# Optimization experiments

Hardware: AMD Instinct MI355X
Metric: run time of the kernel (lower is better)

The kernel has to match this reference:

```python
import jax, jax.numpy as jnp
import numpy as np

B, D, H, W = 64, 64, 32, 32
K = 1024  # num_embeddings


def setup_inputs() -> dict:
    key = jax.random.key(0)
    kx, ke = jax.random.split(key)
    x = jax.random.normal(kx, (B, D, H, W), dtype=jnp.float32)
    # original init: uniform(-sqrt(3), sqrt(3)); randn is fine numerically, but
    # we match the original init distribution for fidelity
    limit = 3.0 ** 0.5
    embedding_table = jax.random.uniform(ke, (D, K), dtype=jnp.float32,
                                         minval=-limit, maxval=limit)
    return {"x": x, "embedding_table": embedding_table}


def reference(x, embedding_table):
    b, d, h, w = x.shape
    flat_x = x.transpose(0, 2, 3, 1).reshape(-1, d)            # [N, D]
    distances = ((flat_x ** 2).sum(1, keepdims=True)
                 - 2.0 * flat_x @ embedding_table
                 + (embedding_table ** 2).sum(0, keepdims=True))  # [N, K]
    encoding_indices = jnp.argmin(distances, axis=1)            # [N]
    quantized = embedding_table.T[encoding_indices]             # [N, D] gather
    quantized = quantized.reshape(b, h, w, d).transpose(0, 3, 1, 2)  # [B,D,H,W]
    dictionary_loss = jnp.mean((jax.lax.stop_gradient(x) - quantized) ** 2)
    commitment_loss = jnp.mean((x - jax.lax.stop_gradient(quantized)) ** 2)
    quantized_st = x + jax.lax.stop_gradient(quantized - x)     # straight-through
    return (quantized_st, dictionary_loss, commitment_loss,
            encoding_indices.reshape(b, -1))
```

## Files before the change

kernel.cpp:

```cpp
#include <hip/hip_runtime.h>


#define DDIM 64
#define KNUM 1024
#define HWN  1024
#define EPS  0.02f

typedef __attribute__((ext_vector_type(8))) short short8v;
typedef __attribute__((ext_vector_type(4))) float f32x4;

__device__ __forceinline__ unsigned short bf16_rn(float v) {
    unsigned u = __float_as_uint(v);
    return (unsigned short)((u + 0x7FFFu + ((u >> 16) & 1u)) >> 16);
}
__device__ __forceinline__ float bf16f(unsigned short h) {
    return __uint_as_float(((unsigned)h) << 16);
}

__global__ __launch_bounds__(256) void vq_convert_e(const float* __restrict__ E,
                                                    float* __restrict__ esq,
                                                    unsigned short* __restrict__ eh,
                                                    unsigned short* __restrict__ el) {
    int k = blockIdx.x * 256 + threadIdx.x;
    float s = 0.f;
    #pragma unroll 8
    for (int d = 0; d < DDIM; ++d) {
        float v = E[d * KNUM + k];
        s = fmaf(v, v, s);
        unsigned short h = bf16_rn(v);
        float lo = v - bf16f(h);
        eh[k * DDIM + d] = h;
        el[k * DDIM + d] = bf16_rn(lo);
    }
    esq[k] = s;
}

__global__ __launch_bounds__(256, 2) void vq_mfma_kernel(const float* __restrict__ x,
                                                         const unsigned short* __restrict__ eh,
                                                         const unsigned short* __restrict__ el,
                                                         const float* __restrict__ esq,
                                                         float* __restrict__ oidx) {
    __shared__ unsigned short blds[2][16384];

    const int t = threadIdx.x;
    const int wv = t >> 6, l = t & 63;
    const int m = l & 15, g = l >> 4;
    const int tileBase = blockIdx.x * 8 + wv * 2;

    const int sr   = wv * 8 + (l >> 3);
    const int sc   = (l & 7) * 16;
    const int scsw = sc ^ ((sr & 7) << 4);
    const unsigned short* srcrow0 =
        (sr < 16) ? (eh + (size_t)sr * DDIM + (scsw >> 1))
                  : (el + (size_t)(sr - 16) * DDIM + (scsw >> 1));
    #define STAGEPH(BUF, P)                                                                  \
        _Pragma("unroll")                                                                    \
        for (int q = 0; q < 8; ++q)                                                          \
            __builtin_amdgcn_global_load_lds(                                                \
                (const __attribute__((address_space(1))) void*)(srcrow0 + (size_t)((P) * 8 + q) * 16 * DDIM), \
                (__attribute__((address_space(3))) void*)&blds[BUF][q * 2048 + wv * 512 + l * 8], \
                16, 0, 0);

    short8v axh[2][2], axl[2][2];
    #pragma unroll
    for (int T = 0; T < 2; ++T) {
        const int n0 = (tileBase + T) * 16;
        const int bb = n0 >> 10, hw0 = n0 & 1023;
        const float* xg = x + (size_t)bb * (DDIM * HWN) + hw0 + m;
        #pragma unroll
        for (int s = 0; s < 2; ++s) {
            #pragma unroll
            for (int i = 0; i < 8; ++i) {
                float v = xg[(s * 32 + g * 8 + i) * HWN];
                unsigned short h = bf16_rn(v);
                axh[T][s][i] = (short)h;
                axl[T][s][i] = (short)bf16_rn(v - bf16f(h));
            }
        }
    }

    const int off_h0 = (m * 128 + (((g * 16)     ) ^ ((m & 7) << 4))) >> 1;
    const int off_h1 = (m * 128 + (((64 + g * 16)) ^ ((m & 7) << 4))) >> 1;
    const int off_l0 = off_h0 + 1024;
    const int off_l1 = off_h1 + 1024;

    float min1[2][4], min2[2][4]; int bk[2][4];
    #pragma unroll
    for (int T = 0; T < 2; ++T)
        #pragma unroll
        for (int j = 0; j < 4; ++j) { min1[T][j] = 3.4e38f; min2[T][j] = 3.4e38f; bk[T][j] = 0; }

    STAGEPH(0, 0);
    __syncthreads();

    for (int p = 0; p < 8; ++p) {
        const int cur = p & 1;
        if (p < 7) STAGEPH(cur ^ 1, p + 1);

        #pragma unroll
        for (int ktl = 0; ktl < 8; ++ktl) {
            const int kt = p * 8 + ktl;
            const unsigned short* bb = &blds[cur][ktl * 2048];
            const short8v bh0 = *reinterpret_cast<const short8v*>(bb + off_h0);
            const short8v bh1 = *reinterpret_cast<const short8v*>(bb + off_h1);
            const short8v bl0 = *reinterpret_cast<const short8v*>(bb + off_l0);
            const short8v bl1 = *reinterpret_cast<const short8v*>(bb + off_l1);
            const float esqv = esq[kt * 16 + m];

            #pragma unroll
            for (int T = 0; T < 2; ++T) {
                f32x4 accA = {0.f, 0.f, 0.f, 0.f};
                f32x4 accB = {0.f, 0.f, 0.f, 0.f};
                accA = __builtin_amdgcn_mfma_f32_16x16x32_bf16(axh[T][0], bh0, accA, 0, 0, 0);
                accA = __builtin_amdgcn_mfma_f32_16x16x32_bf16(axh[T][1], bh1, accA, 0, 0, 0);
                accB = __builtin_amdgcn_mfma_f32_16x16x32_bf16(axh[T][0], bl0, accB, 0, 0, 0);
                accB = __builtin_amdgcn_mfma_f32_16x16x32_bf16(axh[T][1], bl1, accB, 0, 0, 0);
                accA = __builtin_amdgcn_mfma_f32_16x16x32_bf16(axl[T][0], bh0, accA, 0, 0, 0);
                accA = __builtin_amdgcn_mfma_f32_16x16x32_bf16(axl[T][1], bh1, accA, 0, 0, 0);
                #pragma unroll
                for (int j = 0; j < 4; ++j) {
                    float dist = fmaf(-2.f, accA[j] + accB[j], esqv);
                    bool lt = dist < min1[T][j];
                    min2[T][j] = lt ? min1[T][j] : fminf(min2[T][j], dist);
                    bk[T][j]   = lt ? (kt * 16 + m) : bk[T][j];
                    min1[T][j] = lt ? dist          : min1[T][j];
                }
            }
        }
        __syncthreads();
    }
    #undef STAGEPH

    #pragma unroll
    for (int T = 0; T < 2; ++T)
        #pragma unroll
        for (int j = 0; j < 4; ++j) {
            float m1 = min1[T][j], m2 = min2[T][j]; int k1 = bk[T][j];
            #pragma unroll
            for (int off = 8; off >= 1; off >>= 1) {
                float om1 = __shfl_xor(m1, off, 16);
                float om2 = __shfl_xor(m2, off, 16);
                int   ok1 = __shfl_xor(k1, off, 16);
                if (om1 < m1 || (om1 == m1 && ok1 < k1)) {
                    m2 = fminf(m1, om2); m1 = om1; k1 = ok1;
                } else {
                    m2 = fminf(m2, fminf(om1, om2) == om1 ? om2 : om1);
                    m2 = fminf(m2, om1 == m1 ? om2 : om1);
                }
            }
            if (m == j) {
                int n = (tileBase + T) * 16 + g * 4 + j;
                bool flag = (m2 - m1) < EPS;
                oidx[n] = flag ? -(float)(k1 + 1) : (float)k1;
            }
        }
}

__global__ __launch_bounds__(256) void vq_epilogue(const float* __restrict__ x,
                                                   const float* __restrict__ E,
                                                   const float* __restrict__ esq,
                                                   float* __restrict__ oidx,
                                                   float* __restrict__ out_q,
                                                   float* __restrict__ partial) {
    __shared__ float xlds[DDIM * 64];
    __shared__ int   klds[64];
    __shared__ float redlds[4];
    const int t  = threadIdx.x;
    const int wv = t >> 6, ln = t & 63;
    const int n0 = blockIdx.x * 64;
    const int b  = n0 >> 10, hw0 = n0 & 1023;
    const float* xbase = x + (size_t)b * (DDIM * HWN) + hw0;
    #pragma unroll
    for (int it = 0; it < 4; ++it) {
        int dbase = it * 16 + wv * 4;
        int dsub  = ln >> 4;
        int off   = (ln & 15) * 4;
        const float* g = xbase + (dbase + dsub) * HWN + off;
        __builtin_amdgcn_global_load_lds(
            (const __attribute__((address_space(1))) void*)g,
            (__attribute__((address_space(3))) void*)&xlds[dbase * 64 + ln * 4],
            16, 0, 0);
    }
    __syncthreads();
    if (t < 64) klds[t] = (int)oidx[n0 + t];
    __syncthreads();

    for (int r = wv; r < 64; r += 4) {
        if (klds[r] >= 0) continue;
        float acc[16];
        #pragma unroll
        for (int kk = 0; kk < 16; ++kk) acc[kk] = 0.f;
        for (int d = 0; d < DDIM; ++d) {
            float xd = xlds[d * 64 + r];
            #pragma unroll
            for (int kk = 0; kk < 16; ++kk)
                acc[kk] = fmaf(xd, E[d * KNUM + kk * 64 + ln], acc[kk]);
        }
        float bm = 3.4e38f; int bkk = KNUM;
        #pragma unroll
        for (int kk = 0; kk < 16; ++kk) {
            int k = kk * 64 + ln;
            float dist = fmaf(-2.f, acc[kk], esq[k]);
            if (dist < bm) { bm = dist; bkk = k; }
        }
        #pragma unroll
        for (int off = 32; off >= 1; off >>= 1) {
            float ob = __shfl_xor(bm, off);
            int   ok = __shfl_xor(bkk, off);
            if (ob < bm || (ob == bm && ok < bkk)) { bm = ob; bkk = ok; }
        }
        if (ln == 0) { klds[r] = bkk; oidx[n0 + r] = (float)bkk; }
    }
    __syncthreads();

    float lsum = 0.f;
    float* outbase = out_q + (size_t)b * (DDIM * HWN) + hw0;
    #pragma unroll 4
    for (int it = 0; it < 16; ++it) {
        int d = it * 4 + (t >> 6);
        int r = t & 63;
        int k = klds[r];
        float q  = E[d * KNUM + k];
        float xv = xlds[d * 64 + r];
        float diff = xv - q;
        lsum = fmaf(diff, diff, lsum);
        outbase[d * HWN + r] = q;
    }
    #pragma unroll
    for (int off = 32; off >= 1; off >>= 1)
        lsum += __shfl_xor(lsum, off);
    if ((t & 63) == 0) redlds[t >> 6] = lsum;
    __syncthreads();
    if (t == 0)
        partial[blockIdx.x] = (redlds[0] + redlds[1]) + (redlds[2] + redlds[3]);
}

__global__ __launch_bounds__(256) void vq_loss_kernel(const float* __restrict__ partial,
                                                      float* __restrict__ out_loss) {
    __shared__ float red[4];
    int t = threadIdx.x;
    float s = 0.f;
    #pragma unroll
    for (int it = 0; it < 4; ++it) s += partial[it * 256 + t];
    #pragma unroll
    for (int off = 32; off >= 1; off >>= 1) s += __shfl_xor(s, off);
    if ((t & 63) == 0) red[t >> 6] = s;
    __syncthreads();
    if (t == 0) {
        float loss = ((red[0] + red[1]) + (red[2] + red[3])) / 4194304.f;
        out_loss[0] = loss;
        out_loss[1] = loss;
    }
}

extern "C" void kernel_launch(void* const* d_in, const int* in_sizes, int n_in,
                              void* d_out, int out_size, void* d_ws, size_t ws_size,
                              hipStream_t stream) {
    const float* x = (const float*)d_in[0];
    const float* E = (const float*)d_in[1];
    float* out      = (float*)d_out;
    float* out_q    = out;
    float* out_loss = out + 4194304;
    float* oidx     = out + 4194306;

    float* esq     = (float*)d_ws;
    float* partial = esq + 1024;
    unsigned short* eh = (unsigned short*)(partial + 1024);
    unsigned short* el = eh + KNUM * DDIM;

    vq_convert_e<<<4, 256, 0, stream>>>(E, esq, eh, el);
    vq_mfma_kernel<<<512, 256, 0, stream>>>(x, eh, el, esq, oidx);
    vq_epilogue<<<1024, 256, 0, stream>>>(x, E, esq, oidx, out_q, partial);
    vq_loss_kernel<<<1, 256, 0, stream>>>(partial, out_loss);
}
```

Measured before the change: 74.13 us.

## Fuse MFMA distance search with epilogue into one kernel per 64-row block

Merges the MFMA nearest-code search kernel and the epilogue (ambiguous-row fp32 recheck, gather, loss partials) into a single kernel. Each block now handles 64 rows, one 16-row tile per wave. Indices are passed through LDS instead of a global round trip, and the x staging buffer reuses the codebook LDS. The change also halves the LDS stage size, raises the occupancy hint to 4 blocks, and folds the two accumulators into one chain with a branchless min update. The cost is that each wave reuses each codebook tile for one row tile instead of two, so more LDS reads are spent per MFMA.

```diff
diff --git a/kernel.cpp b/kernel.cpp
--- a/kernel.cpp
+++ b/kernel.cpp
@@ -35,46 +35,52 @@
     esq[k] = s;
 }
 
-__global__ __launch_bounds__(256, 2) void vq_mfma_kernel(const float* __restrict__ x,
-                                                         const unsigned short* __restrict__ eh,
-                                                         const unsigned short* __restrict__ el,
-                                                         const float* __restrict__ esq,
-                                                         float* __restrict__ oidx) {
-    __shared__ unsigned short blds[2][16384];
+__global__ __launch_bounds__(256, 4) void vq_mfma_fused(const float* __restrict__ x,
+                                                        const float* __restrict__ E,
+                                                        const unsigned short* __restrict__ eh,
+                                                        const unsigned short* __restrict__ el,
+                                                        const float* __restrict__ esq,
+                                                        float* __restrict__ oidx,
+                                                        float* __restrict__ out_q,
+                                                        float* __restrict__ partial) {
+    __shared__ unsigned short blds[2][8192];
+    __shared__ int   klds[64];
+    __shared__ float redlds[4];
 
     const int t = threadIdx.x;
     const int wv = t >> 6, l = t & 63;
     const int m = l & 15, g = l >> 4;
-    const int tileBase = blockIdx.x * 8 + wv * 2;
-
-    const int sr   = wv * 8 + (l >> 3);
-    const int sc   = (l & 7) * 16;
+    const int tile = blockIdx.x * 4 + wv;
+    const int n0 = blockIdx.x * 64;
+    const int b  = n0 >> 10, hw0 = n0 & 1023;
+
+    const int sr   = t >> 3;
+    const int sc   = (t & 7) * 16;
     const int scsw = sc ^ ((sr & 7) << 4);
     const unsigned short* srcrow0 =
         (sr < 16) ? (eh + (size_t)sr * DDIM + (scsw >> 1))
                   : (el + (size_t)(sr - 16) * DDIM + (scsw >> 1));
     #define STAGEPH(BUF, P)                                                                  \
         _Pragma("unroll")                                                                    \
-        for (int q = 0; q < 8; ++q)                                                          \
+        for (int q = 0; q < 4; ++q)                                                          \
             __builtin_amdgcn_global_load_lds(                                                \
-                (const __attribute__((address_space(1))) void*)(srcrow0 + (size_t)((P) * 8 + q) * 16 * DDIM), \
-                (__attribute__((address_space(3))) void*)&blds[BUF][q * 2048 + wv * 512 + l * 8], \
+                (const __attribute__((address_space(1))) void*)(srcrow0 + (size_t)((P) * 4 + q) * 16 * DDIM), \
+                (__attribute__((address_space(3))) void*)&blds[BUF][q * 2048 + t * 8],       \
                 16, 0, 0);
 
-    short8v axh[2][2], axl[2][2];
-    #pragma unroll
-    for (int T = 0; T < 2; ++T) {
-        const int n0 = (tileBase + T) * 16;
-        const int bb = n0 >> 10, hw0 = n0 & 1023;
-        const float* xg = x + (size_t)bb * (DDIM * HWN) + hw0 + m;
+    short8v axh[2], axl[2];
+    {
+        const int tn0 = tile * 16;
+        const int tb = tn0 >> 10, thw = tn0 & 1023;
+        const float* xg = x + (size_t)tb * (DDIM * HWN) + thw + m;
         #pragma unroll
         for (int s = 0; s < 2; ++s) {
             #pragma unroll
             for (int i = 0; i < 8; ++i) {
                 float v = xg[(s * 32 + g * 8 + i) * HWN];
                 unsigned short h = bf16_rn(v);
-                axh[T][s][i] = (short)h;
-                axl[T][s][i] = (short)bf16_rn(v - bf16f(h));
+                axh[s][i] = (short)h;
+                axl[s][i] = (short)bf16_rn(v - bf16f(h));
             }
         }
     }
@@ -84,22 +90,22 @@
     const int off_l0 = off_h0 + 1024;
     const int off_l1 = off_h1 + 1024;
 
-    float min1[2][4], min2[2][4]; int bk[2][4];
-    #pragma unroll
-    for (int T = 0; T < 2; ++T)
-        #pragma unroll
-        for (int j = 0; j < 4; ++j) { min1[T][j] = 3.4e38f; min2[T][j] = 3.4e38f; bk[T][j] = 0; }
+    float min1[4], min2[4]; int bk[4];
+    #pragma unroll
+    for (int j = 0; j < 4; ++j) { min1[j] = 3.4e38f; min2[j] = 3.4e38f; bk[j] = 0; }
+
+    const f32x4 zf = {0.f, 0.f, 0.f, 0.f};
 
     STAGEPH(0, 0);
     __syncthreads();
 
-    for (int p = 0; p < 8; ++p) {
+    for (int p = 0; p < 16; ++p) {
         const int cur = p & 1;
-        if (p < 7) STAGEPH(cur ^ 1, p + 1);
-
-        #pragma unroll
-        for (int ktl = 0; ktl < 8; ++ktl) {
-            const int kt = p * 8 + ktl;
+        if (p < 15) STAGEPH(cur ^ 1, p + 1);
+
+        #pragma unroll
+        for (int ktl = 0; ktl < 4; ++ktl) {
+            const int kt = p * 4 + ktl;
             const unsigned short* bb = &blds[cur][ktl * 2048];
             const short8v bh0 = *reinterpret_cast<const short8v*>(bb + off_h0);
             const short8v bh1 = *reinterpret_cast<const short8v*>(bb + off_h1);
@@ -107,82 +113,63 @@
             const short8v bl1 = *reinterpret_cast<const short8v*>(bb + off_l1);
             const float esqv = esq[kt * 16 + m];
 
+            f32x4 acc;
+            acc = __builtin_amdgcn_mfma_f32_16x16x32_bf16(axh[0], bh0, zf,  0, 0, 0);
+            acc = __builtin_amdgcn_mfma_f32_16x16x32_bf16(axh[1], bh1, acc, 0, 0, 0);
+            acc = __builtin_amdgcn_mfma_f32_16x16x32_bf16(axh[0], bl0, acc, 0, 0, 0);
+            acc = __builtin_amdgcn_mfma_f32_16x16x32_bf16(axh[1], bl1, acc, 0, 0, 0);
+            acc = __builtin_amdgcn_mfma_f32_16x16x32_bf16(axl[0], bh0, acc, 0, 0, 0);
+            acc = __builtin_amdgcn_mfma_f32_16x16x32_bf16(axl[1], bh1, acc, 0, 0, 0);
+
             #pragma unroll
-            for (int T = 0; T < 2; ++T) {
-                f32x4 accA = {0.f, 0.f, 0.f, 0.f};
-                f32x4 accB = {0.f, 0.f, 0.f, 0.f};
-                accA = __builtin_amdgcn_mfma_f32_16x16x32_bf16(axh[T][0], bh0, accA, 0, 0, 0);
-                accA = __builtin_amdgcn_mfma_f32_16x16x32_bf16(axh[T][1], bh1, accA, 0, 0, 0);
-                accB = __builtin_amdgcn_mfma_f32_16x16x32_bf16(axh[T][0], bl0, accB, 0, 0, 0);
-                accB = __builtin_amdgcn_mfma_f32_16x16x32_bf16(axh[T][1], bl1, accB, 0, 0, 0);
-                accA = __builtin_amdgcn_mfma_f32_16x16x32_bf16(axl[T][0], bh0, accA, 0, 0, 0);
-                accA = __builtin_amdgcn_mfma_f32_16x16x32_bf16(axl[T][1], bh1, accA, 0, 0, 0);
-                #pragma unroll
-                for (int j = 0; j < 4; ++j) {
-                    float dist = fmaf(-2.f, accA[j] + accB[j], esqv);
-                    bool lt = dist < min1[T][j];
-                    min2[T][j] = lt ? min1[T][j] : fminf(min2[T][j], dist);
-                    bk[T][j]   = lt ? (kt * 16 + m) : bk[T][j];
-                    min1[T][j] = lt ? dist          : min1[T][j];
-                }
+            for (int j = 0; j < 4; ++j) {
+                float dist = fmaf(-2.f, acc[j], esqv);
+                min2[j] = fminf(fmaxf(dist, min1[j]), min2[j]);
+                bool lt = dist < min1[j];
+                bk[j]   = lt ? (kt * 16 + m) : bk[j];
+                min1[j] = fminf(min1[j], dist);
             }
         }
         __syncthreads();
     }
     #undef STAGEPH
 
-    #pragma unroll
-    for (int T = 0; T < 2; ++T)
-        #pragma unroll
-        for (int j = 0; j < 4; ++j) {
-            float m1 = min1[T][j], m2 = min2[T][j]; int k1 = bk[T][j];
-            #pragma unroll
-            for (int off = 8; off >= 1; off >>= 1) {
-                float om1 = __shfl_xor(m1, off, 16);
-                float om2 = __shfl_xor(m2, off, 16);
-                int   ok1 = __shfl_xor(k1, off, 16);
-                if (om1 < m1 || (om1 == m1 && ok1 < k1)) {
-                    m2 = fminf(m1, om2); m1 = om1; k1 = ok1;
-                } else {
-                    m2 = fminf(m2, fminf(om1, om2) == om1 ? om2 : om1);
-                    m2 = fminf(m2, om1 == m1 ? om2 : om1);
-                }
+    float* xlds = reinterpret_cast<float*>(&blds[0][0]);
+    {
+        const float* xbase = x + (size_t)b * (DDIM * HWN) + hw0;
+        #pragma unroll
+        for (int it = 0; it < 4; ++it) {
+            int dbase = it * 16 + wv * 4;
+            int dsub  = l >> 4;
+            int off   = (l & 15) * 4;
+            const float* gp = xbase + (dbase + dsub) * HWN + off;
+            __builtin_amdgcn_global_load_lds(
+                (const __attribute__((address_space(1))) void*)gp,
+                (__attribute__((address_space(3))) void*)&xlds[dbase * 64 + l * 4],
+                16, 0, 0);
+        }
+    }
+
+    #pragma unroll
+    for (int j = 0; j < 4; ++j) {
+        float m1 = min1[j], m2 = min2[j]; int k1 = bk[j];
+        #pragma unroll
+        for (int off = 8; off >= 1; off >>= 1) {
+            float om1 = __shfl_xor(m1, off, 16);
+            float om2 = __shfl_xor(m2, off, 16);
+            int   ok1 = __shfl_xor(k1, off, 16);
+            if (om1 < m1 || (om1 == m1 && ok1 < k1)) {
+                m2 = fminf(m1, om2); m1 = om1; k1 = ok1;
+            } else {
+                m2 = fminf(m2, fminf(om1, om2) == om1 ? om2 : om1);
+                m2 = fminf(m2, om1 == m1 ? om2 : om1);
             }
-            if (m == j) {
-                int n = (tileBase + T) * 16 + g * 4 + j;
-                bool flag = (m2 - m1) < EPS;
-                oidx[n] = flag ? -(float)(k1 + 1) : (float)k1;
-            }
-        }
-}
-
-__global__ __launch_bounds__(256) void vq_epilogue(const float* __restrict__ x,
-                                                   const float* __restrict__ E,
-                                                   const float* __restrict__ esq,
-                                                   float* __restrict__ oidx,
-                                                   float* __restrict__ out_q,
-                                                   float* __restrict__ partial) {
-    __shared__ float xlds[DDIM * 64];
-    __shared__ int   klds[64];
-    __shared__ float redlds[4];
-    const int t  = threadIdx.x;
-    const int wv = t >> 6, ln = t & 63;
-    const int n0 = blockIdx.x * 64;
-    const int b  = n0 >> 10, hw0 = n0 & 1023;
-    const float* xbase = x + (size_t)b * (DDIM * HWN) + hw0;
-    #pragma unroll
-    for (int it = 0; it < 4; ++it) {
-        int dbase = it * 16 + wv * 4;
-        int dsub  = ln >> 4;
-        int off   = (ln & 15) * 4;
-        const float* g = xbase + (dbase + dsub) * HWN + off;
-        __builtin_amdgcn_global_load_lds(
-            (const __attribute__((address_space(1))) void*)g,
-            (__attribute__((address_space(3))) void*)&xlds[dbase * 64 + ln * 4],
-            16, 0, 0);
-    }
-    __syncthreads();
-    if (t < 64) klds[t] = (int)oidx[n0 + t];
+        }
+        if (m == j) {
+            int r = wv * 16 + g * 4 + j;
+            klds[r] = (m2 - m1 < EPS) ? -(k1 + 1) : k1;
+        }
+    }
     __syncthreads();
 
     for (int r = wv; r < 64; r += 4) {
@@ -194,12 +181,12 @@
             float xd = xlds[d * 64 + r];
             #pragma unroll
             for (int kk = 0; kk < 16; ++kk)
-                acc[kk] = fmaf(xd, E[d * KNUM + kk * 64 + ln], acc[kk]);
+                acc[kk] = fmaf(xd, E[d * KNUM + kk * 64 + l], acc[kk]);
         }
         float bm = 3.4e38f; int bkk = KNUM;
         #pragma unroll
         for (int kk = 0; kk < 16; ++kk) {
-            int k = kk * 64 + ln;
+            int k = kk * 64 + l;
             float dist = fmaf(-2.f, acc[kk], esq[k]);
             if (dist < bm) { bm = dist; bkk = k; }
         }
@@ -209,7 +196,7 @@
             int   ok = __shfl_xor(bkk, off);
             if (ob < bm || (ob == bm && ok < bkk)) { bm = ob; bkk = ok; }
         }
-        if (ln == 0) { klds[r] = bkk; oidx[n0 + r] = (float)bkk; }
+        if (l == 0) klds[r] = bkk;
     }
     __syncthreads();
 
@@ -226,6 +213,8 @@
         lsum = fmaf(diff, diff, lsum);
         outbase[d * HWN + r] = q;
     }
+    if (t < 64) oidx[n0 + t] = (float)klds[t];
+
     #pragma unroll
     for (int off = 32; off >= 1; off >>= 1)
         lsum += __shfl_xor(lsum, off);
@@ -269,7 +258,6 @@
     unsigned short* el = eh + KNUM * DDIM;
 
     vq_convert_e<<<4, 256, 0, stream>>>(E, esq, eh, el);
-    vq_mfma_kernel<<<512, 256, 0, stream>>>(x, eh, el, esq, oidx);
-    vq_epilogue<<<1024, 256, 0, stream>>>(x, E, esq, oidx, out_q, partial);
+    vq_mfma_fused<<<1024, 256, 0, stream>>>(x, E, eh, el, esq, oidx, out_q, partial);
     vq_loss_kernel<<<1, 256, 0, stream>>>(partial, out_loss);
 }
```

Result: faster. 64.87 us (-12.5%).
